# Performance work log

Measured on AMD Instinct MI355X. Metric: run time of the kernel, lower is better.

## Reference

```python
import jax, jax.numpy as jnp
from jax import lax
import numpy as np

EPS = 1e-3  # Keras BatchNormalization default epsilon

def cond_conv(x, experts, rw, rb):
    # x: [B,H,W,Cin]; experts: [E,kh,kw,Cin,Cout]
    pooled = jnp.mean(x, axis=(1, 2))                       # [B,Cin]
    route = jax.nn.sigmoid(pooled @ rw + rb)                # [B,E]
    kernels = jnp.einsum('be,ehwio->bhwio', route, experts) # per-example kernel
    def conv1(xi, ki):
        return lax.conv_general_dilated(
            xi[None], ki, window_strides=(1, 1), padding='SAME',
            dimension_numbers=('NHWC', 'HWIO', 'NHWC'))[0]
    return jax.vmap(conv1)(x, kernels)

def bn_inf(x, gamma, beta, mean, var):
    inv = gamma * lax.rsqrt(var + EPS)
    return x * inv + (beta - mean * inv)

def maxpool2(x):
    return lax.reduce_window(x, -jnp.inf, lax.max,
                             (1, 2, 2, 1), (1, 2, 2, 1), 'SAME')

def se_block(x, w1, w2):
    s = jnp.mean(x, axis=(1, 2))          # [B,C]
    s = jax.nn.relu(s @ w1)
    s = jax.nn.sigmoid(s @ w2)
    return x * s[:, None, None, :]

def setup_inputs() -> dict:
    key = jax.random.key(0)
    ks = jax.random.split(key, 12)
    d = {
        'x': jax.random.normal(ks[0], (64, 128, 128, 6), jnp.float32),
        'experts1': jax.random.normal(ks[1], (3, 3, 3, 6, 32), jnp.float32) * 0.1,
        'route1_w': jax.random.normal(ks[2], (6, 3), jnp.float32) * 0.1,
        'route1_b': jnp.zeros((3,), jnp.float32),
        'bn1_gamma': jnp.ones((32,), jnp.float32), 'bn1_beta': jnp.zeros((32,), jnp.float32),
        'bn1_mean': jnp.zeros((32,), jnp.float32), 'bn1_var': jnp.ones((32,), jnp.float32),
        'se1_w1': jax.random.normal(ks[3], (32, 2), jnp.float32) * 0.1,
        'se1_w2': jax.random.normal(ks[4], (2, 32), jnp.float32) * 0.1,
        'experts2': jax.random.normal(ks[5], (3, 3, 3, 32, 64), jnp.float32) * 0.05,
        'route2_w': jax.random.normal(ks[6], (32, 3), jnp.float32) * 0.1,
        'route2_b': jnp.zeros((3,), jnp.float32),
        'bn2_gamma': jnp.ones((64,), jnp.float32), 'bn2_beta': jnp.zeros((64,), jnp.float32),
        'bn2_mean': jnp.zeros((64,), jnp.float32), 'bn2_var': jnp.ones((64,), jnp.float32),
        'se2_w1': jax.random.normal(ks[7], (64, 4), jnp.float32) * 0.1,
        'se2_w2': jax.random.normal(ks[8], (4, 64), jnp.float32) * 0.1,
        'experts3': jax.random.normal(ks[9], (3, 3, 3, 64, 128), jnp.float32) * 0.05,
        'route3_w': jax.random.normal(ks[10], (64, 3), jnp.float32) * 0.1,
        'route3_b': jnp.zeros((3,), jnp.float32),
        'bn3_gamma': jnp.ones((128,), jnp.float32), 'bn3_beta': jnp.zeros((128,), jnp.float32),
        'bn3_mean': jnp.zeros((128,), jnp.float32), 'bn3_var': jnp.ones((128,), jnp.float32),
    }
    return d

def reference(x, experts1, route1_w, route1_b, bn1_gamma, bn1_beta, bn1_mean, bn1_var,
              se1_w1, se1_w2, experts2, route2_w, route2_b, bn2_gamma, bn2_beta,
              bn2_mean, bn2_var, se2_w1, se2_w2, experts3, route3_w, route3_b,
              bn3_gamma, bn3_beta, bn3_mean, bn3_var):
    h = cond_conv(x, experts1, route1_w, route1_b)
    h = jax.nn.relu(bn_inf(h, bn1_gamma, bn1_beta, bn1_mean, bn1_var))
    h = maxpool2(h)                       # [B,64,64,32]
    h = se_block(h, se1_w1, se1_w2)
    h = cond_conv(h, experts2, route2_w, route2_b)
    h = jax.nn.relu(bn_inf(h, bn2_gamma, bn2_beta, bn2_mean, bn2_var))
    h = maxpool2(h)                       # [B,32,32,64]
    h = se_block(h, se2_w1, se2_w2)
    h = cond_conv(h, experts3, route3_w, route3_b)
    h = bn_inf(h, bn3_gamma, bn3_beta, bn3_mean, bn3_var)
    return jnp.mean(h, axis=(1, 2))       # [B,128]
```

## Files before the change

### kernel.cpp

```cpp
#include <hip/hip_runtime.h>

#define EPSBN 1e-3f

typedef unsigned short ushort_t;
typedef __attribute__((ext_vector_type(8))) short bf8;
typedef __attribute__((ext_vector_type(4))) float f4;

__device__ __forceinline__ float sigmoidf_(float z) {
  return 1.0f / (1.0f + expf(-z));
}

__device__ __forceinline__ ushort_t f2bf(float x) {
  union { float f; unsigned u; } v; v.f = x;
  unsigned r = (v.u + 0x7fffu + ((v.u >> 16) & 1u)) >> 16;
  return (ushort_t)r;
}

__global__ void k_mean_x(const float* __restrict__ x, float* __restrict__ part,
                         float* __restrict__ S_agg, unsigned* __restrict__ done) {
  const int b = blockIdx.x >> 2;
  const int q = blockIdx.x & 3;
  const int tid = threadIdx.x;
  if (tid < 144) S_agg[(size_t)b * 576 + q * 144 + tid] = 0.0f;
  if (q == 0 && tid == 0) done[b] = 0u;

  float acc[6] = {0.f, 0.f, 0.f, 0.f, 0.f, 0.f};
  const float* xb = x + (size_t)b * 98304 + (size_t)q * 24576;
  for (int p = 0; p < 4; ++p) {
    const float* base = xb + (size_t)p * 6144 + (size_t)tid * 24;
#pragma unroll
    for (int k = 0; k < 6; ++k) {
      const float4 v = *(const float4*)(base + k * 4);
      acc[(4 * k + 0) % 6] += v.x;
      acc[(4 * k + 1) % 6] += v.y;
      acc[(4 * k + 2) % 6] += v.z;
      acc[(4 * k + 3) % 6] += v.w;
    }
  }
#pragma unroll
  for (int c = 0; c < 6; ++c)
    for (int off = 32; off > 0; off >>= 1) acc[c] += __shfl_down(acc[c], off, 64);
  __shared__ float red[4][6];
  const int lane = tid & 63, w = tid >> 6;
  if (lane == 0) {
#pragma unroll
    for (int c = 0; c < 6; ++c) red[w][c] = acc[c];
  }
  __syncthreads();
  if (tid < 6) {
    part[blockIdx.x * 6 + tid] = red[0][tid] + red[1][tid] + red[2][tid] + red[3][tid];
  }
}

__global__ __launch_bounds__(256)
void k_conv1(const float* __restrict__ x, const float* __restrict__ meanx_part,
             const float* __restrict__ experts1,
             const float* __restrict__ rw, const float* __restrict__ rbias,
             const float* __restrict__ gamma, const float* __restrict__ beta,
             const float* __restrict__ bnmean, const float* __restrict__ bnvar,
             ushort_t* __restrict__ p1b, float* __restrict__ part_m1) {
  const int bid = blockIdx.x;
  const int b = bid >> 3;
  const int tyi = (bid >> 1) & 3;
  const int txi = bid & 1;
  __shared__ __align__(16) ushort_t patch[34 * 68 * 8];
  __shared__ float route_s[3];
  __shared__ float mred[4][32];
  const int tid = threadIdx.x;
  const float* xb = x + (size_t)b * (128 * 128 * 6);

  if (tid < 3) {
    float z = rbias[tid];
    for (int c = 0; c < 6; ++c) {
      const float s = meanx_part[(b * 4 + 0) * 6 + c] + meanx_part[(b * 4 + 1) * 6 + c] +
                      meanx_part[(b * 4 + 2) * 6 + c] + meanx_part[(b * 4 + 3) * 6 + c];
      z += (s * (1.0f / 16384.0f)) * rw[c * 3 + tid];
    }
    route_s[tid] = sigmoidf_(z);
  }

  for (int v = tid; v < 34 * 68; v += 256) {
    const int ry = v / 68, p = v - ry * 68;
    const int gy = tyi * 32 - 1 + ry, gx = txi * 64 - 1 + p;
    uint4 u = make_uint4(0u, 0u, 0u, 0u);
    if (((unsigned)gy < 128u) && ((unsigned)gx < 128u)) {
      const float* s = xb + ((size_t)(gy * 128 + gx)) * 6;
      const float2 a0 = *(const float2*)s;
      const float2 a1 = *(const float2*)(s + 2);
      const float2 a2 = *(const float2*)(s + 4);
      u.x = (unsigned)f2bf(a0.x) | ((unsigned)f2bf(a0.y) << 16);
      u.y = (unsigned)f2bf(a1.x) | ((unsigned)f2bf(a1.y) << 16);
      u.z = (unsigned)f2bf(a2.x) | ((unsigned)f2bf(a2.y) << 16);
      u.w = 0u;
    }
    *(uint4*)(patch + (size_t)v * 8) = u;
  }
  __syncthreads();

  const int w = tid >> 6;
  const int lane = tid & 63;
  const int lx = lane & 15, lg = lane >> 4;

  const float r0 = route_s[0], r1 = route_s[1], r2 = route_s[2];
  const int co0 = lx, co1 = 16 + lx;
  const float inv0 = gamma[co0] * rsqrtf(bnvar[co0] + EPSBN);
  const float bias0 = beta[co0] - bnmean[co0] * inv0;
  const float inv1 = gamma[co1] * rsqrtf(bnvar[co1] + EPSBN);
  const float bias1 = beta[co1] - bnmean[co1] * inv1;

  bf8 Bf[3][2];
#pragma unroll
  for (int ky = 0; ky < 3; ++ky) {
#pragma unroll
    for (int nt = 0; nt < 2; ++nt) {
      const int co = nt * 16 + lx;
      const float inv = nt ? inv1 : inv0;
#pragma unroll
      for (int j = 0; j < 8; ++j) {
        float val = 0.f;
        if (j < 6 && lg < 3) {
          const int idx = ((ky * 3 + lg) * 6 + j) * 32 + co;
          val = (r0 * experts1[idx] + r1 * experts1[1728 + idx] +
                 r2 * experts1[3456 + idx]) * inv;
        }
        Bf[ky][nt][j] = (short)f2bf(val);
      }
    }
  }

  float msum0 = 0.f, msum1 = 0.f;
#pragma unroll
  for (int xt = 0; xt < 4; ++xt) {
    bf8 Af[10];
#pragma unroll
    for (int r = 0; r < 10; ++r)
      Af[r] = *(const bf8*)(patch + ((size_t)(w * 8 + r) * 68 + xt * 16 + lx + lg) * 8);
#pragma unroll
    for (int rp = 0; rp < 4; ++rp) {
      const int prow = tyi * 16 + w * 4 + rp;
      f4 acc0[2], acc1[2];
#pragma unroll
      for (int nt = 0; nt < 2; ++nt) {
        acc0[nt] = (f4){0.f, 0.f, 0.f, 0.f};
        acc1[nt] = (f4){0.f, 0.f, 0.f, 0.f};
      }
#pragma unroll
      for (int ky = 0; ky < 3; ++ky) {
#pragma unroll
        for (int nt = 0; nt < 2; ++nt) {
          acc0[nt] = __builtin_amdgcn_mfma_f32_16x16x32_bf16(Af[rp * 2 + ky], Bf[ky][nt], acc0[nt], 0, 0, 0);
          acc1[nt] = __builtin_amdgcn_mfma_f32_16x16x32_bf16(Af[rp * 2 + ky + 1], Bf[ky][nt], acc1[nt], 0, 0, 0);
        }
      }
#pragma unroll
      for (int nt = 0; nt < 2; ++nt) {
        const float bias = nt ? bias1 : bias0;
        const int co = nt * 16 + lx;
#pragma unroll
        for (int q = 0; q < 2; ++q) {
          const float m0 = fmaxf(acc0[nt][2 * q] + bias, 0.f);
          const float m1 = fmaxf(acc0[nt][2 * q + 1] + bias, 0.f);
          const float m2 = fmaxf(acc1[nt][2 * q] + bias, 0.f);
          const float m3 = fmaxf(acc1[nt][2 * q + 1] + bias, 0.f);
          const float mx = fmaxf(fmaxf(m0, m1), fmaxf(m2, m3));
          if (nt) msum1 += mx; else msum0 += mx;
          const int pcol = txi * 32 + xt * 8 + lg * 2 + q;
          p1b[(((size_t)b * 64 + prow) * 64 + pcol) * 32 + co] = f2bf(mx);
        }
      }
    }
  }

  msum0 += __shfl_xor(msum0, 16, 64);
  msum0 += __shfl_xor(msum0, 32, 64);
  msum1 += __shfl_xor(msum1, 16, 64);
  msum1 += __shfl_xor(msum1, 32, 64);
  if (lg == 0) {
    mred[w][lx] = msum0;
    mred[w][16 + lx] = msum1;
  }
  __syncthreads();
  if (tid < 32) {
    part_m1[(size_t)bid * 32 + tid] =
        mred[0][tid] + mred[1][tid] + mred[2][tid] + mred[3][tid];
  }
}

__global__ __launch_bounds__(256)
void k_conv2f(const ushort_t* __restrict__ p1b, const float* __restrict__ part_m1,
              const float* __restrict__ experts2,
              const float* __restrict__ rw2, const float* __restrict__ rb2,
              const float* __restrict__ sw1a, const float* __restrict__ sw1b,
              const float* __restrict__ g2, const float* __restrict__ be2,
              const float* __restrict__ mu2, const float* __restrict__ va2,
              const float* __restrict__ experts3,
              const float* __restrict__ rw3, const float* __restrict__ rb3,
              const float* __restrict__ sw2a, const float* __restrict__ sw2b,
              const float* __restrict__ g3, const float* __restrict__ be3,
              const float* __restrict__ mu3, const float* __restrict__ va3,
              float* __restrict__ S_agg, unsigned* __restrict__ done,
              float* __restrict__ out) {
  const int bi = blockIdx.x;
  const int b = bi >> 5;
  const int ti = bi & 31;
  const int tile = ti >> 1, cog = ti & 1;
  const int ty = tile >> 2, tx2 = tile & 3;
  __shared__ __align__(16) unsigned char smem[53568];
  __shared__ int is_last;
  short* As = (short*)smem;
  short* Bs = As + 12960;
  float* aux = (float*)(smem + 48960);
  const int tid = threadIdx.x;

  const ushort_t* pb = p1b + (size_t)b * 131072;
  for (int v = tid; v < 1296; v += 256) {
    const int cell = v >> 2, part = v & 3;
    const int ly = cell / 18, lx2 = cell - ly * 18;
    const int gy = ty * 16 - 1 + ly, gx = tx2 * 16 - 1 + lx2;
    uint4 d = make_uint4(0u, 0u, 0u, 0u);
    if (((unsigned)gy < 64u) && ((unsigned)gx < 64u))
      d = *(const uint4*)(pb + (((size_t)gy << 6) + gx) * 32 + part * 8);
    *(uint4*)(As + (ly * 18 + lx2) * 40 + part * 8) = d;
  }

  float* m1 = aux;
  float* h = aux + 32;
  float* s1 = aux + 36;
  float* route = aux + 68;
  if (tid < 32) {
    float s = 0.f;
#pragma unroll
    for (int k = 0; k < 8; ++k) s += part_m1[(size_t)(b * 8 + k) * 32 + tid];
    m1[tid] = s * (1.0f / 4096.0f);
  }
  __syncthreads();
  if (tid < 2) {
    float z = 0.f;
    for (int c = 0; c < 32; ++c) z += m1[c] * sw1a[c * 2 + tid];
    h[tid] = fmaxf(z, 0.f);
  }
  __syncthreads();
  if (tid < 32) s1[tid] = sigmoidf_(h[0] * sw1b[tid] + h[1] * sw1b[32 + tid]);
  __syncthreads();
  if (tid < 3) {
    float z = rb2[tid];
    for (int c = 0; c < 32; ++c) z += m1[c] * s1[c] * rw2[c * 3 + tid];
    route[tid] = sigmoidf_(z);
  }
  __syncthreads();

  const float r0 = route[0], r1 = route[1], r2 = route[2];
  const int n_l = tid & 31;
  const int co_g = cog * 32 + n_l;
  const float inv2c = g2[co_g] * rsqrtf(va2[co_g] + EPSBN);
  for (int j = 0; j < 36; ++j) {
    const int idx = j * 256 + tid;
    const int ci = (idx >> 5) & 31;
    const int tap = idx >> 10;
    const int t = (tap * 32 + ci) * 64 + co_g;
    const float v = r0 * experts2[t] + r1 * experts2[18432 + t] + r2 * experts2[36864 + t];
    Bs[(tap * 32 + n_l) * 40 + ci] = (short)f2bf(v * s1[ci] * inv2c);
  }
  __syncthreads();

  const int w = tid >> 6;
  const int lane = tid & 63;
  const int lx = lane & 15, lg = lane >> 4;

  f4 acc[4][2];
#pragma unroll
  for (int mt = 0; mt < 4; ++mt)
#pragma unroll
    for (int nt = 0; nt < 2; ++nt)
      acc[mt][nt] = (f4){0.f, 0.f, 0.f, 0.f};

#pragma unroll
  for (int kx = 0; kx < 3; ++kx) {
    bf8 Af[6];
#pragma unroll
    for (int r = 0; r < 6; ++r)
      Af[r] = *(const bf8*)(As + ((4 * w + r) * 18 + lx + kx) * 40 + (lg << 3));
#pragma unroll
    for (int ky = 0; ky < 3; ++ky) {
      const int t = ky * 3 + kx;
      const bf8 Bf0 = *(const bf8*)(Bs + ((t << 5) + lx) * 40 + (lg << 3));
      const bf8 Bf1 = *(const bf8*)(Bs + ((t << 5) + 16 + lx) * 40 + (lg << 3));
#pragma unroll
      for (int mt = 0; mt < 4; ++mt) {
        acc[mt][0] = __builtin_amdgcn_mfma_f32_16x16x32_bf16(Af[ky + mt], Bf0, acc[mt][0], 0, 0, 0);
        acc[mt][1] = __builtin_amdgcn_mfma_f32_16x16x32_bf16(Af[ky + mt], Bf1, acc[mt][1], 0, 0, 0);
      }
    }
  }

  float inv[2], bias[2];
#pragma unroll
  for (int nt = 0; nt < 2; ++nt) {
    const int co = cog * 32 + nt * 16 + lx;
    inv[nt] = g2[co] * rsqrtf(va2[co] + EPSBN);
    bias[nt] = be2[co] - mu2[co] * inv[nt];
  }
  float agg[2][9];
#pragma unroll
  for (int nt = 0; nt < 2; ++nt)
#pragma unroll
    for (int a = 0; a < 9; ++a) agg[nt][a] = 0.f;

#pragma unroll
  for (int half = 0; half < 2; ++half) {
    const int prow = ty * 8 + 2 * w + half;
    const bool rT = (prow == 0), rB = (prow == 31);
#pragma unroll
    for (int q = 0; q < 2; ++q) {
      const int pcol = tx2 * 8 + 2 * lg + q;
      const bool cL = (pcol == 0), cR = (pcol == 31);
#pragma unroll
      for (int nt = 0; nt < 2; ++nt) {
        const float m0 = fmaxf(acc[2 * half][nt][2 * q] + bias[nt], 0.f);
        const float m1 = fmaxf(acc[2 * half][nt][2 * q + 1] + bias[nt], 0.f);
        const float m2 = fmaxf(acc[2 * half + 1][nt][2 * q] + bias[nt], 0.f);
        const float m3 = fmaxf(acc[2 * half + 1][nt][2 * q + 1] + bias[nt], 0.f);
        const float mx = fmaxf(fmaxf(m0, m1), fmaxf(m2, m3));
        agg[nt][0] += mx;
        if (rT) agg[nt][1] += mx;
        if (rB) agg[nt][2] += mx;
        if (cL) agg[nt][3] += mx;
        if (cR) agg[nt][4] += mx;
        if (rT && cL) agg[nt][5] += mx;
        if (rT && cR) agg[nt][6] += mx;
        if (rB && cL) agg[nt][7] += mx;
        if (rB && cR) agg[nt][8] += mx;
      }
    }
  }

#pragma unroll
  for (int nt = 0; nt < 2; ++nt)
#pragma unroll
    for (int a = 0; a < 9; ++a) {
      float v = agg[nt][a];
      v += __shfl_xor(v, 16, 64);
      v += __shfl_xor(v, 32, 64);
      agg[nt][a] = v;
    }
  float* sred = aux;
  if (lg == 0) {
#pragma unroll
    for (int nt = 0; nt < 2; ++nt)
#pragma unroll
      for (int a = 0; a < 9; ++a)
        sred[((w * 2 + nt) * 16 + lx) * 9 + a] = agg[nt][a];
  }
  __syncthreads();
  for (int v = tid; v < 288; v += 256) {
    const int a = v >> 5;
    const int colocal = v & 31;
    const int nt = colocal >> 4, lxx = colocal & 15;
    float s = 0.f;
#pragma unroll
    for (int ww = 0; ww < 4; ++ww) s += sred[((ww * 2 + nt) * 16 + lxx) * 9 + a];
    atomicAdd(&S_agg[(size_t)b * 576 + a * 64 + cog * 32 + colocal], s);
  }

  __syncthreads();
  if (tid == 0) {
    const unsigned old = atomicAdd(&done[b], 1u);
    is_last = (old == 31u) ? 1 : 0;
  }
  __syncthreads();
  if (!is_last) return;

  float* AG = (float*)smem;
  float* Sp = AG + 576;
  float* m2 = Sp + 576;
  float* hh = m2 + 64;
  float* s2 = hh + 4;
  float* rt = s2 + 64;
  float* redf = rt + 4;
  for (int v = tid; v < 576; v += 256)
    AG[v] = atomicAdd(&S_agg[(size_t)b * 576 + v], 0.0f);
  __syncthreads();
  if (tid < 64) m2[tid] = AG[tid] * (1.0f / 1024.0f);
  __syncthreads();
  if (tid < 4) {
    float z = 0.f;
    for (int c = 0; c < 64; ++c) z += m2[c] * sw2a[c * 4 + tid];
    hh[tid] = fmaxf(z, 0.f);
  }
  __syncthreads();
  if (tid < 64) {
    float z = 0.f;
#pragma unroll
    for (int j = 0; j < 4; ++j) z += hh[j] * sw2b[j * 64 + tid];
    s2[tid] = sigmoidf_(z);
  }
  __syncthreads();
  if (tid < 3) {
    float z = rb3[tid];
    for (int c = 0; c < 64; ++c) z += m2[c] * s2[c] * rw3[c * 3 + tid];
    rt[tid] = sigmoidf_(z);
  }
  __syncthreads();
  for (int v = tid; v < 576; v += 256) {
    const int tap = v >> 6, ci = v & 63;
    const int ky = tap / 3, kx = tap - 3 * ky;
    const float T = AG[ci];
    const float A = (ky == 0) ? AG[2 * 64 + ci] : ((ky == 2) ? AG[1 * 64 + ci] : 0.f);
    const float B = (kx == 0) ? AG[4 * 64 + ci] : ((kx == 2) ? AG[3 * 64 + ci] : 0.f);
    float AB = 0.f;
    if (ky == 0 && kx == 0) AB = AG[8 * 64 + ci];
    else if (ky == 0 && kx == 2) AB = AG[7 * 64 + ci];
    else if (ky == 2 && kx == 0) AB = AG[6 * 64 + ci];
    else if (ky == 2 && kx == 2) AB = AG[5 * 64 + ci];
    Sp[tap * 64 + ci] = (T - A - B + AB) * s2[ci];
  }
  __syncthreads();

  const int co = tid & 127;
  const int hf = tid >> 7;
  const int tap_lo = hf ? 5 : 0;
  const int tap_hi = hf ? 9 : 5;
  float acc2 = 0.f;
#pragma unroll
  for (int e = 0; e < 3; ++e) {
    float m = 0.f;
    for (int tap = tap_lo; tap < tap_hi; ++tap) {
      const float* E = experts3 + ((size_t)(e * 9 + tap) * 64) * 128 + co;
#pragma unroll 16
      for (int ci = 0; ci < 64; ++ci) m = fmaf(E[(size_t)ci * 128], Sp[tap * 64 + ci], m);
    }
    acc2 += rt[e] * m;
  }
  redf[hf * 128 + co] = acc2;
  __syncthreads();
  if (tid < 128) {
    const float total = redf[tid] + redf[128 + tid];
    const float invf = g3[tid] * rsqrtf(va3[tid] + EPSBN);
    out[(size_t)b * 128 + tid] = total * (1.0f / 1024.0f) * invf + (be3[tid] - mu3[tid] * invf);
  }
}

extern "C" void kernel_launch(void* const* d_in, const int* in_sizes, int n_in,
                              void* d_out, int out_size, void* d_ws, size_t ws_size,
                              hipStream_t stream) {
  const float* x        = (const float*)d_in[0];
  const float* experts1 = (const float*)d_in[1];
  const float* rw1      = (const float*)d_in[2];
  const float* rb1      = (const float*)d_in[3];
  const float* g1  = (const float*)d_in[4];
  const float* be1 = (const float*)d_in[5];
  const float* mu1 = (const float*)d_in[6];
  const float* va1 = (const float*)d_in[7];
  const float* sw1a = (const float*)d_in[8];
  const float* sw1b = (const float*)d_in[9];
  const float* experts2 = (const float*)d_in[10];
  const float* rw2 = (const float*)d_in[11];
  const float* rb2 = (const float*)d_in[12];
  const float* g2  = (const float*)d_in[13];
  const float* be2 = (const float*)d_in[14];
  const float* mu2 = (const float*)d_in[15];
  const float* va2 = (const float*)d_in[16];
  const float* sw2a = (const float*)d_in[17];
  const float* sw2b = (const float*)d_in[18];
  const float* experts3 = (const float*)d_in[19];
  const float* rw3 = (const float*)d_in[20];
  const float* rb3 = (const float*)d_in[21];
  const float* g3  = (const float*)d_in[22];
  const float* be3 = (const float*)d_in[23];
  const float* mu3 = (const float*)d_in[24];
  const float* va3 = (const float*)d_in[25];
  float* out = (float*)d_out;
  float* ws = (float*)d_ws;

  float* meanx_part = ws;
  float* part_m1    = ws + 1536;
  float* S_agg      = ws + 17920;
  unsigned* done    = (unsigned*)(ws + 54784);
  ushort_t* p1b     = (ushort_t*)(ws + 54848);

  hipLaunchKernelGGL(k_mean_x, dim3(256), dim3(256), 0, stream, x, meanx_part, S_agg, done);
  hipLaunchKernelGGL(k_conv1, dim3(512), dim3(256), 0, stream,
                     x, meanx_part, experts1, rw1, rb1, g1, be1, mu1, va1, p1b, part_m1);
  hipLaunchKernelGGL(k_conv2f, dim3(2048), dim3(256), 0, stream,
                     p1b, part_m1, experts2, rw2, rb2, sw1a, sw1b, g2, be2, mu2, va2,
                     experts3, rw3, rb3, sw2a, sw2b, g3, be3, mu3, va3,
                     S_agg, done, out);
}
```

Measured before the change: 214.7 us.

## Precompute per-example conv2 kernels in a separate kernel instead of per block

Adds a k_buildk2 kernel that computes the SE/routing scalars and the mixed, BN-scaled bf16 conv2 weights once per example, stored in a workspace buffer in the conv layout. k_conv2f then just copies its 32-column slice of weights into shared memory with vector loads, instead of each of the 32 blocks per example redoing the routing math and the 3-expert weight mix from fp32. This removes redundant weight-generation work and serial sync steps, and shrinks shared memory. The cost is an extra kernel launch and a global round trip of the weights.

```diff
diff --git a/kernel.cpp b/kernel.cpp
--- a/kernel.cpp
+++ b/kernel.cpp
@@ -186,11 +186,51 @@
   }
 }
 
+__global__ void k_buildk2(const float* __restrict__ part_m1,
+                          const float* __restrict__ experts2,
+                          const float* __restrict__ rw, const float* __restrict__ rb,
+                          const float* __restrict__ w1, const float* __restrict__ w2,
+                          const float* __restrict__ gamma, const float* __restrict__ var,
+                          ushort_t* __restrict__ k2pb) {
+  const int b = blockIdx.x / 3;
+  const int seg = blockIdx.x - b * 3;
+  const int tid = threadIdx.x;
+  __shared__ float m1[32], h[2], s1[32], route[3];
+  if (tid < 32) {
+    float s = 0.f;
+#pragma unroll
+    for (int k = 0; k < 8; ++k) s += part_m1[(size_t)(b * 8 + k) * 32 + tid];
+    m1[tid] = s * (1.0f / 4096.0f);
+  }
+  __syncthreads();
+  if (tid < 2) {
+    float z = 0.f;
+    for (int c = 0; c < 32; ++c) z += m1[c] * w1[c * 2 + tid];
+    h[tid] = fmaxf(z, 0.f);
+  }
+  __syncthreads();
+  if (tid < 32) s1[tid] = sigmoidf_(h[0] * w2[tid] + h[1] * w2[32 + tid]);
+  __syncthreads();
+  if (tid < 3) {
+    float z = rb[tid];
+    for (int c = 0; c < 32; ++c) z += m1[c] * s1[c] * rw[c * 3 + tid];
+    route[tid] = sigmoidf_(z);
+  }
+  __syncthreads();
+  const float r0 = route[0], r1 = route[1], r2 = route[2];
+  const int t_lo = seg * 6144, t_hi = t_lo + 6144;
+  for (int t = t_lo + tid; t < t_hi; t += 256) {
+    const int co = t & 63;
+    const int ci = (t >> 6) & 31;
+    const int tap = t >> 11;
+    const float inv = gamma[co] * rsqrtf(var[co] + EPSBN);
+    const float v = r0 * experts2[t] + r1 * experts2[18432 + t] + r2 * experts2[2 * 18432 + t];
+    k2pb[(size_t)b * 18432 + ((size_t)tap * 64 + co) * 32 + ci] = f2bf(v * s1[ci] * inv);
+  }
+}
+
 __global__ __launch_bounds__(256)
-void k_conv2f(const ushort_t* __restrict__ p1b, const float* __restrict__ part_m1,
-              const float* __restrict__ experts2,
-              const float* __restrict__ rw2, const float* __restrict__ rb2,
-              const float* __restrict__ sw1a, const float* __restrict__ sw1b,
+void k_conv2f(const ushort_t* __restrict__ p1b, const ushort_t* __restrict__ k2pb,
               const float* __restrict__ g2, const float* __restrict__ be2,
               const float* __restrict__ mu2, const float* __restrict__ va2,
               const float* __restrict__ experts3,
@@ -202,14 +242,13 @@
               float* __restrict__ out) {
   const int bi = blockIdx.x;
   const int b = bi >> 5;
-  const int ti = bi & 31;
-  const int tile = ti >> 1, cog = ti & 1;
+  const int tile = (bi >> 1) & 15;
+  const int cog = bi & 1;
   const int ty = tile >> 2, tx2 = tile & 3;
-  __shared__ __align__(16) unsigned char smem[53568];
+  __shared__ __align__(16) short smem[24480];
   __shared__ int is_last;
-  short* As = (short*)smem;
-  short* Bs = As + 12960;
-  float* aux = (float*)(smem + 48960);
+  short* As = smem;
+  short* Bs = smem + 12960;
   const int tid = threadIdx.x;
 
   const ushort_t* pb = p1b + (size_t)b * 131072;
@@ -222,44 +261,12 @@
       d = *(const uint4*)(pb + (((size_t)gy << 6) + gx) * 32 + part * 8);
     *(uint4*)(As + (ly * 18 + lx2) * 40 + part * 8) = d;
   }
-
-  float* m1 = aux;
-  float* h = aux + 32;
-  float* s1 = aux + 36;
-  float* route = aux + 68;
-  if (tid < 32) {
-    float s = 0.f;
-#pragma unroll
-    for (int k = 0; k < 8; ++k) s += part_m1[(size_t)(b * 8 + k) * 32 + tid];
-    m1[tid] = s * (1.0f / 4096.0f);
-  }
-  __syncthreads();
-  if (tid < 2) {
-    float z = 0.f;
-    for (int c = 0; c < 32; ++c) z += m1[c] * sw1a[c * 2 + tid];
-    h[tid] = fmaxf(z, 0.f);
-  }
-  __syncthreads();
-  if (tid < 32) s1[tid] = sigmoidf_(h[0] * sw1b[tid] + h[1] * sw1b[32 + tid]);
-  __syncthreads();
-  if (tid < 3) {
-    float z = rb2[tid];
-    for (int c = 0; c < 32; ++c) z += m1[c] * s1[c] * rw2[c * 3 + tid];
-    route[tid] = sigmoidf_(z);
-  }
-  __syncthreads();
-
-  const float r0 = route[0], r1 = route[1], r2 = route[2];
-  const int n_l = tid & 31;
-  const int co_g = cog * 32 + n_l;
-  const float inv2c = g2[co_g] * rsqrtf(va2[co_g] + EPSBN);
-  for (int j = 0; j < 36; ++j) {
-    const int idx = j * 256 + tid;
-    const int ci = (idx >> 5) & 31;
-    const int tap = idx >> 10;
-    const int t = (tap * 32 + ci) * 64 + co_g;
-    const float v = r0 * experts2[t] + r1 * experts2[18432 + t] + r2 * experts2[36864 + t];
-    Bs[(tap * 32 + n_l) * 40 + ci] = (short)f2bf(v * s1[ci] * inv2c);
+  for (int v = tid; v < 1152; v += 256) {
+    const int r = v >> 2, part = v & 3;
+    const int t = r >> 5, n = r & 31;
+    const uint4 d = *(const uint4*)(k2pb + (size_t)b * 18432 +
+                                    ((size_t)(t * 64 + cog * 32 + n)) * 32 + part * 8);
+    *(uint4*)(Bs + r * 40 + part * 8) = d;
   }
   __syncthreads();
 
@@ -343,7 +350,8 @@
       v += __shfl_xor(v, 32, 64);
       agg[nt][a] = v;
     }
-  float* sred = aux;
+  __syncthreads();
+  float* sred = (float*)smem;
   if (lg == 0) {
 #pragma unroll
     for (int nt = 0; nt < 2; ++nt)
@@ -476,13 +484,16 @@
   float* part_m1    = ws + 1536;
   float* S_agg      = ws + 17920;
   unsigned* done    = (unsigned*)(ws + 54784);
-  ushort_t* p1b     = (ushort_t*)(ws + 54848);
+  ushort_t* k2pb    = (ushort_t*)(ws + 54848);
+  ushort_t* p1b     = (ushort_t*)(ws + 644672);
 
   hipLaunchKernelGGL(k_mean_x, dim3(256), dim3(256), 0, stream, x, meanx_part, S_agg, done);
   hipLaunchKernelGGL(k_conv1, dim3(512), dim3(256), 0, stream,
                      x, meanx_part, experts1, rw1, rb1, g1, be1, mu1, va1, p1b, part_m1);
+  hipLaunchKernelGGL(k_buildk2, dim3(192), dim3(256), 0, stream,
+                     part_m1, experts2, rw2, rb2, sw1a, sw1b, g2, va2, k2pb);
   hipLaunchKernelGGL(k_conv2f, dim3(2048), dim3(256), 0, stream,
-                     p1b, part_m1, experts2, rw2, rb2, sw1a, sw1b, g2, be2, mu2, va2,
+                     p1b, k2pb, g2, be2, mu2, va2,
                      experts3, rw3, rb3, sw2a, sw2b, g3, be3, mu3, va3,
                      S_agg, done, out);
 }
```

After: 213.1 us. About the same (-0.8%).
